# Optimization experiments

Hardware: AMD Instinct MI355X
Metric: run time of the kernel (lower is better)

The kernel has to match this reference:

```python
import jax, jax.numpy as jnp
import numpy as np
from jax import lax

N_HEAD = 16
SEQ = 2048
EMB = 512
D = SEQ // N_HEAD  # input_dim = 128
KSIZE = 3
EPS = 1e-5  # BatchNorm1d default eps


def setup_inputs() -> dict:
    key = jax.random.key(0)
    ks = jax.random.split(key, 5)
    inputs = jax.random.normal(ks[0], (8, SEQ, EMB), jnp.float32)
    # grouped Conv1d: groups = D, weight shape (out_ch, in_ch/groups, k) = (512, 4, 3)
    conv_w = jax.random.normal(ks[1], (EMB, EMB // D, KSIZE), jnp.float32) * 0.1
    conv_b = jax.random.normal(ks[2], (EMB,), jnp.float32) * 0.1
    gamma = jnp.ones((EMB,), jnp.float32)
    beta = jnp.zeros((EMB,), jnp.float32)
    lin_w = jax.random.normal(ks[3], (D, D), jnp.float32) * (1.0 / np.sqrt(D))
    lin_b = jax.random.normal(ks[4], (D,), jnp.float32) * 0.1
    return {"inputs": inputs, "conv_w": conv_w, "conv_b": conv_b,
            "gamma": gamma, "beta": beta, "lin_w": lin_w, "lin_b": lin_b}


def reference(inputs, conv_w, conv_b, gamma, beta, lin_w, lin_b):
    b = inputs.shape[0]
    # nlp mode: (b, S, E) -> (b*n_head, E, D)
    x = inputs.reshape(-1, EMB, D)

    # local information: grouped Conv1d (stride 1, padding 1, groups=D) + residual, GELU, BatchNorm (training stats)
    conv = lax.conv_general_dilated(
        x, conv_w, window_strides=(1,), padding=[(1, 1)],
        dimension_numbers=("NCH", "OIH", "NCH"), feature_group_count=D,
    ) + conv_b[None, :, None]
    q = jax.nn.gelu(conv + x, approximate=False)
    mu = q.mean(axis=(0, 2), keepdims=True)
    var = q.var(axis=(0, 2), keepdims=True)  # biased, as torch BN uses for normalization
    q = gamma[None, :, None] * (q - mu) * lax.rsqrt(var + EPS) + beta[None, :, None]

    # bernoulli sampling with prob=1 -> all-ones mask -> plain softmax over dim=-2 (the E axis)
    k = jax.nn.gelu(jax.nn.softmax(x, axis=1), approximate=False)

    # global information: Linear(D, D) on last dim, then GELU
    v = jax.nn.gelu(jnp.einsum("bed,od->beo", x, lin_w) + lin_b, approximate=False)

    # attention: (B', E, D) x (B', D, E) -> (B', E, E), softmax over last dim
    attn = jax.nn.softmax(
        jnp.einsum("bed,bfd->bef", q, k) / np.float32(np.sqrt(EMB)), axis=-1
    )
    out = jnp.einsum("bef,bfd->bed", attn, v)  # (B', E, D)
    return out.reshape(b, SEQ, EMB), attn
```

## Files before the change

### kernel.cpp

```cpp
#include <hip/hip_runtime.h>
#include <math.h>

#define Bn   128
#define Ech  512
#define Dd   128
#define NCNT 16384

typedef __bf16 bf16;
typedef __attribute__((ext_vector_type(8))) __bf16 bf16x8;
typedef __attribute__((ext_vector_type(4))) __bf16 bf16x4;
typedef __attribute__((ext_vector_type(4))) float f32x4;

__device__ __forceinline__ float gelu_exact(float x) {
    return 0.5f * x * (1.0f + erff(x * 0.70710678118654752f));
}

static __device__ __forceinline__ f32x4 mfma16(bf16x8 a, bf16x8 b, f32x4 c) {
    return __builtin_amdgcn_mfma_f32_16x16x32_bf16(a, b, c, 0, 0, 0);
}

#define SWZ(byte, row) ((unsigned)(byte) ^ (((unsigned)(row) & 7u) << 4))

__global__ __launch_bounds__(256) void k_conv_gelu_stats(
    const float* __restrict__ x, const float* __restrict__ cw,
    const float* __restrict__ cb, bf16* __restrict__ qpre,
    float* __restrict__ csum, float* __restrict__ csumsq)
{
    __shared__ float xt[64 * 128];
    const int n  = blockIdx.y;
    const int c0 = blockIdx.x * 64;
    const float* xb = x + (size_t)n * Ech * Dd + (size_t)c0 * Dd;

    const float4* xb4 = (const float4*)xb;
    float4* xt4 = (float4*)xt;
    #pragma unroll
    for (int j = 0; j < 8; j++) xt4[threadIdx.x + 256 * j] = xb4[threadIdx.x + 256 * j];
    __syncthreads();

    const int oloc = threadIdx.x >> 2;
    const int hq   = threadIdx.x & 3;
    const int o    = c0 + oloc;
    const int gb   = oloc & ~3;

    float w[4][3];
    #pragma unroll
    for (int i = 0; i < 4; i++)
        #pragma unroll
        for (int kk = 0; kk < 3; kk++) w[i][kk] = cw[o * 12 + i * 3 + kk];
    const float bias = cb[o];

    float s = 0.f, ss = 0.f;
    bf16* qrow = qpre + (size_t)n * Ech * Dd + (size_t)o * Dd;
    #pragma unroll 4
    for (int j = 0; j < 32; j++) {
        const int h = hq + 4 * j;
        float acc = bias;
        #pragma unroll
        for (int i = 0; i < 4; i++) {
            const float* row = &xt[(gb + i) * 128];
            const float xm = (h > 0)   ? row[h - 1] : 0.f;
            const float xc = row[h];
            const float xp = (h < 127) ? row[h + 1] : 0.f;
            acc = fmaf(xm, w[i][0], acc);
            acc = fmaf(xc, w[i][1], acc);
            acc = fmaf(xp, w[i][2], acc);
        }
        acc += xt[oloc * 128 + h];
        const float g = gelu_exact(acc);
        qrow[h] = (bf16)g;
        s += g; ss = fmaf(g, g, ss);
    }
    s  += __shfl_xor(s, 1);  s  += __shfl_xor(s, 2);
    ss += __shfl_xor(ss, 1); ss += __shfl_xor(ss, 2);
    if (hq == 0) { atomicAdd(&csum[o], s); atomicAdd(&csumsq[o], ss); }
}

__global__ void k_stats_final(const float* __restrict__ csum,
                              const float* __restrict__ csumsq,
                              const float* __restrict__ gamma,
                              const float* __restrict__ beta,
                              float* __restrict__ scale, float* __restrict__ shift)
{
    const int c = threadIdx.x;
    if (c < Ech) {
        const float mu   = csum[c]   * (1.0f / NCNT);
        const float var  = csumsq[c] * (1.0f / NCNT) - mu * mu;
        const float rstd = rsqrtf(var + 1e-5f);
        const float sc   = gamma[c] * rstd;
        scale[c] = sc;
        shift[c] = beta[c] - mu * sc;
    }
}

__global__ __launch_bounds__(256) void k_softmax_e_gelu_v2(
    const float* __restrict__ x, bf16* __restrict__ kout)
{
    __shared__ float4 red[32][8];
    const int n  = blockIdx.y;
    const int qd = blockIdx.x;
    const int t  = threadIdx.x;
    const int d4 = t & 7;
    const int eg = t >> 3;
    const float* xb = x + (size_t)n * Ech * Dd + qd * 32 + d4 * 4;

    float4 vb[16];
    float4 m4 = {-3e38f, -3e38f, -3e38f, -3e38f};
    #pragma unroll
    for (int j = 0; j < 16; j++) {
        const int e = eg + 32 * j;
        float4 v = *(const float4*)(xb + (size_t)e * Dd);
        vb[j] = v;
        m4.x = fmaxf(m4.x, v.x); m4.y = fmaxf(m4.y, v.y);
        m4.z = fmaxf(m4.z, v.z); m4.w = fmaxf(m4.w, v.w);
    }
    red[eg][d4] = m4;
    __syncthreads();
    #pragma unroll
    for (int s = 16; s >= 1; s >>= 1) {
        if (eg < s) {
            float4 a = red[eg][d4], b = red[eg + s][d4];
            a.x = fmaxf(a.x, b.x); a.y = fmaxf(a.y, b.y);
            a.z = fmaxf(a.z, b.z); a.w = fmaxf(a.w, b.w);
            red[eg][d4] = a;
        }
        __syncthreads();
    }
    m4 = red[0][d4];
    __syncthreads();

    float4 s4 = {0.f, 0.f, 0.f, 0.f};
    #pragma unroll
    for (int j = 0; j < 16; j++) {
        float4 v = vb[j];
        v.x = __expf(v.x - m4.x); v.y = __expf(v.y - m4.y);
        v.z = __expf(v.z - m4.z); v.w = __expf(v.w - m4.w);
        vb[j] = v;
        s4.x += v.x; s4.y += v.y; s4.z += v.z; s4.w += v.w;
    }
    red[eg][d4] = s4;
    __syncthreads();
    #pragma unroll
    for (int s = 16; s >= 1; s >>= 1) {
        if (eg < s) {
            float4 a = red[eg][d4], b = red[eg + s][d4];
            a.x += b.x; a.y += b.y; a.z += b.z; a.w += b.w;
            red[eg][d4] = a;
        }
        __syncthreads();
    }
    s4 = red[0][d4];
    const float4 inv4 = {1.0f / s4.x, 1.0f / s4.y, 1.0f / s4.z, 1.0f / s4.w};

    bf16* kb = kout + (size_t)n * Ech * Dd + qd * 32 + d4 * 4;
    #pragma unroll
    for (int j = 0; j < 16; j++) {
        const int e = eg + 32 * j;
        float4 p = vb[j];
        bf16x4 ov;
        ov[0] = (bf16)gelu_exact(p.x * inv4.x);
        ov[1] = (bf16)gelu_exact(p.y * inv4.y);
        ov[2] = (bf16)gelu_exact(p.z * inv4.z);
        ov[3] = (bf16)gelu_exact(p.w * inv4.w);
        *(bf16x4*)(kb + (size_t)e * Dd) = ov;
    }
}

__global__ __launch_bounds__(256) void k_vgemm_T(
    const float* __restrict__ x, const float* __restrict__ lw,
    const float* __restrict__ lb, bf16* __restrict__ vT)
{
    __shared__ bf16 As[64 * 128];
    __shared__ bf16 Bs[64 * 128];
    const int n = blockIdx.z, e0 = blockIdx.x * 64, o0 = blockIdx.y * 64;
    const int t = threadIdx.x, lane = t & 63, w = t >> 6;
    const int wr = w >> 1, wc = w & 1;
    const int lr = lane & 15, lg = lane >> 4;

    {
        const float* sa = lw + (size_t)o0 * Dd;
        const float* sb = x + (size_t)n * Ech * Dd + (size_t)e0 * Dd;
        #pragma unroll
        for (int p = 0; p < 4; p++) {
            const int idx = t + 256 * p;
            const int row = idx >> 4, k16 = idx & 15;
            float4 a0 = *(const float4*)(sa + (size_t)row * Dd + k16 * 8);
            float4 a1 = *(const float4*)(sa + (size_t)row * Dd + k16 * 8 + 4);
            bf16x8 oa;
            oa[0]=(bf16)a0.x; oa[1]=(bf16)a0.y; oa[2]=(bf16)a0.z; oa[3]=(bf16)a0.w;
            oa[4]=(bf16)a1.x; oa[5]=(bf16)a1.y; oa[6]=(bf16)a1.z; oa[7]=(bf16)a1.w;
            *(bf16x8*)((char*)As + SWZ(row * 256 + k16 * 16, row)) = oa;
            float4 b0 = *(const float4*)(sb + (size_t)row * Dd + k16 * 8);
            float4 b1 = *(const float4*)(sb + (size_t)row * Dd + k16 * 8 + 4);
            bf16x8 ob;
            ob[0]=(bf16)b0.x; ob[1]=(bf16)b0.y; ob[2]=(bf16)b0.z; ob[3]=(bf16)b0.w;
            ob[4]=(bf16)b1.x; ob[5]=(bf16)b1.y; ob[6]=(bf16)b1.z; ob[7]=(bf16)b1.w;
            *(bf16x8*)((char*)Bs + SWZ(row * 256 + k16 * 16, row)) = ob;
        }
    }
    __syncthreads();

    f32x4 acc[2][2] = {};
    #pragma unroll
    for (int ks = 0; ks < 4; ks++) {
        const int ko = ks * 32 + lg * 8;
        const int ra0 = wr * 32 + lr, ra1 = wr * 32 + 16 + lr;
        const int rb0 = wc * 32 + lr, rb1 = wc * 32 + 16 + lr;
        const bf16x8 a0 = *(const bf16x8*)((char*)As + SWZ(ra0 * 256 + ko * 2, ra0));
        const bf16x8 a1 = *(const bf16x8*)((char*)As + SWZ(ra1 * 256 + ko * 2, ra1));
        const bf16x8 b0 = *(const bf16x8*)((char*)Bs + SWZ(rb0 * 256 + ko * 2, rb0));
        const bf16x8 b1 = *(const bf16x8*)((char*)Bs + SWZ(rb1 * 256 + ko * 2, rb1));
        acc[0][0] = mfma16(a0, b0, acc[0][0]);
        acc[0][1] = mfma16(a0, b1, acc[0][1]);
        acc[1][0] = mfma16(a1, b0, acc[1][0]);
        acc[1][1] = mfma16(a1, b1, acc[1][1]);
    }

    bf16* vb = vT + (size_t)n * Dd * Ech;
    #pragma unroll
    for (int mm = 0; mm < 2; mm++) {
        #pragma unroll
        for (int nn = 0; nn < 2; nn++) {
            const int ecol = e0 + wc * 32 + nn * 16 + lr;
            #pragma unroll
            for (int r4 = 0; r4 < 4; r4++) {
                const int orow = o0 + wr * 32 + mm * 16 + lg * 4 + r4;
                vb[(size_t)orow * Ech + ecol] =
                    (bf16)gelu_exact(acc[mm][nn][r4] + lb[orow]);
            }
        }
    }
}

#define QS_OFF 0
#define KS_OFF 16384
#define PS_OFF 16384
#define VS_OFF 81920
#define LDS_TOTAL 147456

__global__ __launch_bounds__(256) void k_attn_fused(
    const bf16* __restrict__ qpre, const bf16* __restrict__ kbuf,
    const bf16* __restrict__ vT, const float* __restrict__ scale,
    const float* __restrict__ shift, float* __restrict__ attn,
    float* __restrict__ out)
{
    __shared__ char lds[LDS_TOTAL];
    const int n = blockIdx.y, e0 = blockIdx.x * 64;
    const int t = threadIdx.x, lane = t & 63, w = t >> 6;
    const int lr = lane & 15, lg = lane >> 4;

    {
        const bf16* src = qpre + (size_t)n * Ech * Dd + (size_t)e0 * Dd;
        #pragma unroll
        for (int p = 0; p < 4; p++) {
            const int idx = t + 256 * p;
            const int row = idx >> 4, k16 = idx & 15;
            bf16x8 v = *(const bf16x8*)(src + row * Dd + k16 * 8);
            const float sc = scale[e0 + row], sh = shift[e0 + row];
            bf16x8 o;
            #pragma unroll
            for (int j = 0; j < 8; j++) o[j] = (bf16)fmaf((float)v[j], sc, sh);
            *(bf16x8*)(lds + QS_OFF + SWZ(row * 256 + k16 * 16, row)) = o;
        }
    }
    {
        const bf16* src = kbuf + (size_t)n * Ech * Dd;
        #pragma unroll
        for (int p = 0; p < 32; p++) {
            const int idx = t + 256 * p;
            const int row = idx >> 4, k16 = idx & 15;
            float4 v = *(const float4*)(src + row * Dd + k16 * 8);
            *(float4*)(lds + KS_OFF + SWZ(row * 256 + k16 * 16, row)) = v;
        }
    }
    __syncthreads();

    f32x4 acc[32];
    #pragma unroll
    for (int i = 0; i < 32; i++) acc[i] = (f32x4){0.f, 0.f, 0.f, 0.f};
    #pragma unroll
    for (int ks = 0; ks < 4; ks++) {
        const int arow = w * 16 + lr;
        const int ko = ks * 32 + lg * 8;
        const bf16x8 a = *(const bf16x8*)(lds + QS_OFF + SWZ(arow * 256 + ko * 2, arow));
        #pragma unroll
        for (int ft = 0; ft < 32; ft++) {
            const int brow = ft * 16 + lr;
            const bf16x8 b = *(const bf16x8*)(lds + KS_OFF + SWZ(brow * 256 + ko * 2, brow));
            acc[ft] = mfma16(a, b, acc[ft]);
        }
    }
    __syncthreads();

    const float rsc = 0.044194173824159216f;
    float m[4] = {-3e38f, -3e38f, -3e38f, -3e38f};
    #pragma unroll
    for (int ft = 0; ft < 32; ft++)
        #pragma unroll
        for (int r4 = 0; r4 < 4; r4++) m[r4] = fmaxf(m[r4], acc[ft][r4]);
    #pragma unroll
    for (int off = 1; off <= 8; off <<= 1)
        #pragma unroll
        for (int r4 = 0; r4 < 4; r4++) m[r4] = fmaxf(m[r4], __shfl_xor(m[r4], off));

    float s[4] = {0.f, 0.f, 0.f, 0.f};
    #pragma unroll
    for (int ft = 0; ft < 32; ft++)
        #pragma unroll
        for (int r4 = 0; r4 < 4; r4++) {
            const float p = __expf((acc[ft][r4] - m[r4]) * rsc);
            acc[ft][r4] = p;
            s[r4] += p;
        }
    #pragma unroll
    for (int off = 1; off <= 8; off <<= 1)
        #pragma unroll
        for (int r4 = 0; r4 < 4; r4++) s[r4] += __shfl_xor(s[r4], off);
    float inv[4];
    #pragma unroll
    for (int r4 = 0; r4 < 4; r4++) inv[r4] = 1.0f / s[r4];

    #pragma unroll
    for (int ft = 0; ft < 32; ft++)
        #pragma unroll
        for (int r4 = 0; r4 < 4; r4++) {
            const int row = w * 16 + lg * 4 + r4;
            const int col = ft * 16 + lr;
            *(bf16*)(lds + PS_OFF + SWZ(row * 1024 + col * 2, row)) =
                (bf16)(acc[ft][r4] * inv[r4]);
        }

    const bf16* vsrc = vT + (size_t)n * Dd * Ech;
    #pragma unroll
    for (int p = 0; p < 16; p++) {
        const int idx = t + 256 * p;
        const int row = idx >> 5, c16 = idx & 31;
        float4 v = *(const float4*)(vsrc + (size_t)row * Ech + c16 * 8);
        *(float4*)(lds + VS_OFF + SWZ(row * 512 + c16 * 16, row)) = v;
    }
    __syncthreads();

    f32x4 acc2[8];
    #pragma unroll
    for (int i = 0; i < 8; i++) acc2[i] = (f32x4){0.f, 0.f, 0.f, 0.f};
    #pragma unroll
    for (int kf = 0; kf < 8; kf++) {
        const int arow = w * 16 + lr;
        const int fcol = kf * 32 + lg * 8;
        const bf16x8 a = *(const bf16x8*)(lds + PS_OFF + SWZ(arow * 1024 + fcol * 2, arow));
        #pragma unroll
        for (int dt = 0; dt < 8; dt++) {
            const int brow = dt * 16 + lr;
            const bf16x8 b = *(const bf16x8*)(lds + VS_OFF + SWZ(brow * 512 + fcol * 2, brow));
            acc2[dt] = mfma16(a, b, acc2[dt]);
        }
    }

    {
        float* ab = attn + (size_t)n * Ech * Ech + (size_t)e0 * Ech;
        #pragma unroll
        for (int p = 0; p < 32; p++) {
            const int idx = t + 256 * p;
            const int row = idx >> 7, c4 = idx & 127;
            bf16x4 pv = *(const bf16x4*)(lds + PS_OFF + SWZ(row * 1024 + c4 * 8, row));
            float4 o = {(float)pv[0], (float)pv[1], (float)pv[2], (float)pv[3]};
            *(float4*)(ab + (size_t)row * Ech + c4 * 4) = o;
        }
    }
    __syncthreads();

    #pragma unroll
    for (int p = 0; p < 16; p++) {
        const int idx = t + 256 * p;
        const int row = idx >> 5, c16 = idx & 31;
        float4 v = *(const float4*)(vsrc + (size_t)row * Ech + 256 + c16 * 8);
        *(float4*)(lds + VS_OFF + SWZ(row * 512 + c16 * 16, row)) = v;
    }
    __syncthreads();

    #pragma unroll
    for (int kf = 0; kf < 8; kf++) {
        const int arow = w * 16 + lr;
        const int fcol = 256 + kf * 32 + lg * 8;
        const bf16x8 a = *(const bf16x8*)(lds + PS_OFF + SWZ(arow * 1024 + fcol * 2, arow));
        #pragma unroll
        for (int dt = 0; dt < 8; dt++) {
            const int brow = dt * 16 + lr;
            const int vcol = kf * 32 + lg * 8;
            const bf16x8 b = *(const bf16x8*)(lds + VS_OFF + SWZ(brow * 512 + vcol * 2, brow));
            acc2[dt] = mfma16(a, b, acc2[dt]);
        }
    }

    float* ob = out + (size_t)n * Ech * Dd;
    #pragma unroll
    for (int dt = 0; dt < 8; dt++)
        #pragma unroll
        for (int r4 = 0; r4 < 4; r4++) {
            const int erow = e0 + w * 16 + lg * 4 + r4;
            const int dcol = dt * 16 + lr;
            ob[(size_t)erow * Dd + dcol] = acc2[dt][r4];
        }
}

extern "C" void kernel_launch(void* const* d_in, const int* in_sizes, int n_in,
                              void* d_out, int out_size, void* d_ws, size_t ws_size,
                              hipStream_t stream)
{
    const float* x     = (const float*)d_in[0];
    const float* cw    = (const float*)d_in[1];
    const float* cb    = (const float*)d_in[2];
    const float* gamma = (const float*)d_in[3];
    const float* beta  = (const float*)d_in[4];
    const float* lw    = (const float*)d_in[5];
    const float* lb    = (const float*)d_in[6];

    float* out  = (float*)d_out;
    float* attn = out + (size_t)8388608;

    bf16*  qpre_bf = (bf16*)d_ws;
    bf16*  kb_bf   = qpre_bf + 8388608;
    bf16*  vT_bf   = kb_bf + 8388608;
    float* csum    = (float*)(vT_bf + 8388608);
    float* csumsq  = csum + 512;
    float* scale   = csumsq + 512;
    float* shift   = scale + 512;

    hipMemsetAsync(csum, 0, 2 * 512 * sizeof(float), stream);

    k_conv_gelu_stats<<<dim3(8, 128), 256, 0, stream>>>(x, cw, cb, qpre_bf, csum, csumsq);
    k_stats_final<<<1, 512, 0, stream>>>(csum, csumsq, gamma, beta, scale, shift);
    k_softmax_e_gelu_v2<<<dim3(4, 128), 256, 0, stream>>>(x, kb_bf);
    k_vgemm_T<<<dim3(8, 2, 128), 256, 0, stream>>>(x, lw, lb, vT_bf);
    k_attn_fused<<<dim3(8, 128), 256, 0, stream>>>(
        qpre_bf, kb_bf, vT_bf, scale, shift, attn, out);
}
```

Baseline: 310.6 us.

## Restructure fused attention kernel into 2x2 warp tiling with smaller LDS footprint

The fused attention kernel now splits its four warps into a 2x2 grid. Each warp keeps its Q fragments in registers, streams K in two 256-row chunks, and merges softmax row max and sum across the two column-warps through a small LDS exchange. P reuses the K buffer, and V is streamed in 64-column chunks, which cuts LDS from 144KB to 80KB so more blocks can be resident per CU. In exchange the kernel has more barriers, a cross-warp softmax reduction, and loads Q directly from global memory.

```diff
diff --git a/kernel.cpp b/kernel.cpp
--- a/kernel.cpp
+++ b/kernel.cpp
@@ -231,129 +231,151 @@
     }
 }
 
-#define QS_OFF 0
-#define KS_OFF 16384
-#define PS_OFF 16384
-#define VS_OFF 81920
-#define LDS_TOTAL 147456
-
-__global__ __launch_bounds__(256) void k_attn_fused(
+#define KP_OFF  0
+#define SMR_OFF 65536
+#define VC_OFF  65536
+#define ATT_LDS 81920
+
+__global__ __launch_bounds__(256) void k_attn_fused2(
     const bf16* __restrict__ qpre, const bf16* __restrict__ kbuf,
     const bf16* __restrict__ vT, const float* __restrict__ scale,
     const float* __restrict__ shift, float* __restrict__ attn,
     float* __restrict__ out)
 {
-    __shared__ char lds[LDS_TOTAL];
+    __shared__ char lds[ATT_LDS];
     const int n = blockIdx.y, e0 = blockIdx.x * 64;
     const int t = threadIdx.x, lane = t & 63, w = t >> 6;
+    const int wr = w >> 1, wc = w & 1;
     const int lr = lane & 15, lg = lane >> 4;
 
-    {
-        const bf16* src = qpre + (size_t)n * Ech * Dd + (size_t)e0 * Dd;
-        #pragma unroll
-        for (int p = 0; p < 4; p++) {
+    bf16x8 qa[2][4];
+    #pragma unroll
+    for (int rt = 0; rt < 2; rt++) {
+        const int row = e0 + wr * 32 + rt * 16 + lr;
+        const float sc = scale[row], sh = shift[row];
+        const bf16* qr = qpre + (size_t)n * Ech * Dd + (size_t)row * Dd + lg * 8;
+        #pragma unroll
+        for (int ks = 0; ks < 4; ks++) {
+            bf16x8 v = *(const bf16x8*)(qr + ks * 32);
+            bf16x8 o;
+            #pragma unroll
+            for (int j = 0; j < 8; j++) o[j] = (bf16)fmaf((float)v[j], sc, sh);
+            qa[rt][ks] = o;
+        }
+    }
+
+    f32x4 acc[2][16];
+    #pragma unroll
+    for (int rt = 0; rt < 2; rt++)
+        #pragma unroll
+        for (int j = 0; j < 16; j++) acc[rt][j] = (f32x4){0.f, 0.f, 0.f, 0.f};
+
+    const bf16* kb = kbuf + (size_t)n * Ech * Dd;
+    #pragma unroll
+    for (int c = 0; c < 2; c++) {
+        __syncthreads();
+        #pragma unroll
+        for (int p = 0; p < 16; p++) {
             const int idx = t + 256 * p;
             const int row = idx >> 4, k16 = idx & 15;
-            bf16x8 v = *(const bf16x8*)(src + row * Dd + k16 * 8);
-            const float sc = scale[e0 + row], sh = shift[e0 + row];
-            bf16x8 o;
-            #pragma unroll
-            for (int j = 0; j < 8; j++) o[j] = (bf16)fmaf((float)v[j], sc, sh);
-            *(bf16x8*)(lds + QS_OFF + SWZ(row * 256 + k16 * 16, row)) = o;
-        }
-    }
-    {
-        const bf16* src = kbuf + (size_t)n * Ech * Dd;
-        #pragma unroll
-        for (int p = 0; p < 32; p++) {
-            const int idx = t + 256 * p;
-            const int row = idx >> 4, k16 = idx & 15;
-            float4 v = *(const float4*)(src + row * Dd + k16 * 8);
-            *(float4*)(lds + KS_OFF + SWZ(row * 256 + k16 * 16, row)) = v;
-        }
-    }
-    __syncthreads();
-
-    f32x4 acc[32];
-    #pragma unroll
-    for (int i = 0; i < 32; i++) acc[i] = (f32x4){0.f, 0.f, 0.f, 0.f};
-    #pragma unroll
-    for (int ks = 0; ks < 4; ks++) {
-        const int arow = w * 16 + lr;
-        const int ko = ks * 32 + lg * 8;
-        const bf16x8 a = *(const bf16x8*)(lds + QS_OFF + SWZ(arow * 256 + ko * 2, arow));
-        #pragma unroll
-        for (int ft = 0; ft < 32; ft++) {
-            const int brow = ft * 16 + lr;
-            const bf16x8 b = *(const bf16x8*)(lds + KS_OFF + SWZ(brow * 256 + ko * 2, brow));
-            acc[ft] = mfma16(a, b, acc[ft]);
-        }
-    }
-    __syncthreads();
+            float4 v = *(const float4*)(kb + (size_t)(c * 256 + row) * Dd + k16 * 8);
+            *(float4*)(lds + KP_OFF + SWZ(row * 256 + k16 * 16, row)) = v;
+        }
+        __syncthreads();
+        #pragma unroll
+        for (int ks = 0; ks < 4; ks++)
+            #pragma unroll
+            for (int ct = 0; ct < 8; ct++) {
+                const int brow = wc * 128 + ct * 16 + lr;
+                const bf16x8 b = *(const bf16x8*)(lds + KP_OFF +
+                                   SWZ(brow * 256 + ks * 64 + lg * 16, brow));
+                acc[0][c * 8 + ct] = mfma16(qa[0][ks], b, acc[0][c * 8 + ct]);
+                acc[1][c * 8 + ct] = mfma16(qa[1][ks], b, acc[1][c * 8 + ct]);
+            }
+    }
 
     const float rsc = 0.044194173824159216f;
-    float m[4] = {-3e38f, -3e38f, -3e38f, -3e38f};
-    #pragma unroll
-    for (int ft = 0; ft < 32; ft++)
-        #pragma unroll
-        for (int r4 = 0; r4 < 4; r4++) m[r4] = fmaxf(m[r4], acc[ft][r4]);
+    float mloc[2][4], sloc[2][4];
+    #pragma unroll
+    for (int rt = 0; rt < 2; rt++)
+        #pragma unroll
+        for (int r4 = 0; r4 < 4; r4++) mloc[rt][r4] = -3e38f;
+    #pragma unroll
+    for (int rt = 0; rt < 2; rt++)
+        #pragma unroll
+        for (int j = 0; j < 16; j++)
+            #pragma unroll
+            for (int r4 = 0; r4 < 4; r4++)
+                mloc[rt][r4] = fmaxf(mloc[rt][r4], acc[rt][j][r4]);
     #pragma unroll
     for (int off = 1; off <= 8; off <<= 1)
         #pragma unroll
-        for (int r4 = 0; r4 < 4; r4++) m[r4] = fmaxf(m[r4], __shfl_xor(m[r4], off));
-
-    float s[4] = {0.f, 0.f, 0.f, 0.f};
-    #pragma unroll
-    for (int ft = 0; ft < 32; ft++)
+        for (int rt = 0; rt < 2; rt++)
+            #pragma unroll
+            for (int r4 = 0; r4 < 4; r4++)
+                mloc[rt][r4] = fmaxf(mloc[rt][r4], __shfl_xor(mloc[rt][r4], off));
+
+    #pragma unroll
+    for (int rt = 0; rt < 2; rt++)
+        #pragma unroll
+        for (int r4 = 0; r4 < 4; r4++) sloc[rt][r4] = 0.f;
+    #pragma unroll
+    for (int rt = 0; rt < 2; rt++)
+        #pragma unroll
+        for (int j = 0; j < 16; j++)
+            #pragma unroll
+            for (int r4 = 0; r4 < 4; r4++) {
+                const float p = __expf((acc[rt][j][r4] - mloc[rt][r4]) * rsc);
+                acc[rt][j][r4] = p;
+                sloc[rt][r4] += p;
+            }
+    #pragma unroll
+    for (int off = 1; off <= 8; off <<= 1)
+        #pragma unroll
+        for (int rt = 0; rt < 2; rt++)
+            #pragma unroll
+            for (int r4 = 0; r4 < 4; r4++)
+                sloc[rt][r4] += __shfl_xor(sloc[rt][r4], off);
+
+    float* pmax = (float*)(lds + SMR_OFF);
+    float* psum = (float*)(lds + SMR_OFF + 512);
+    if (lr == 0) {
+        #pragma unroll
+        for (int rt = 0; rt < 2; rt++)
+            #pragma unroll
+            for (int r4 = 0; r4 < 4; r4++) {
+                const int row = wr * 32 + rt * 16 + lg * 4 + r4;
+                pmax[wc * 64 + row] = mloc[rt][r4];
+                psum[wc * 64 + row] = sloc[rt][r4];
+            }
+    }
+    __syncthreads();
+
+    float fac[2][4];
+    #pragma unroll
+    for (int rt = 0; rt < 2; rt++)
         #pragma unroll
         for (int r4 = 0; r4 < 4; r4++) {
-            const float p = __expf((acc[ft][r4] - m[r4]) * rsc);
-            acc[ft][r4] = p;
-            s[r4] += p;
-        }
-    #pragma unroll
-    for (int off = 1; off <= 8; off <<= 1)
-        #pragma unroll
-        for (int r4 = 0; r4 < 4; r4++) s[r4] += __shfl_xor(s[r4], off);
-    float inv[4];
-    #pragma unroll
-    for (int r4 = 0; r4 < 4; r4++) inv[r4] = 1.0f / s[r4];
-
-    #pragma unroll
-    for (int ft = 0; ft < 32; ft++)
-        #pragma unroll
-        for (int r4 = 0; r4 < 4; r4++) {
-            const int row = w * 16 + lg * 4 + r4;
-            const int col = ft * 16 + lr;
-            *(bf16*)(lds + PS_OFF + SWZ(row * 1024 + col * 2, row)) =
-                (bf16)(acc[ft][r4] * inv[r4]);
-        }
-
-    const bf16* vsrc = vT + (size_t)n * Dd * Ech;
-    #pragma unroll
-    for (int p = 0; p < 16; p++) {
-        const int idx = t + 256 * p;
-        const int row = idx >> 5, c16 = idx & 31;
-        float4 v = *(const float4*)(vsrc + (size_t)row * Ech + c16 * 8);
-        *(float4*)(lds + VS_OFF + SWZ(row * 512 + c16 * 16, row)) = v;
-    }
-    __syncthreads();
-
-    f32x4 acc2[8];
-    #pragma unroll
-    for (int i = 0; i < 8; i++) acc2[i] = (f32x4){0.f, 0.f, 0.f, 0.f};
-    #pragma unroll
-    for (int kf = 0; kf < 8; kf++) {
-        const int arow = w * 16 + lr;
-        const int fcol = kf * 32 + lg * 8;
-        const bf16x8 a = *(const bf16x8*)(lds + PS_OFF + SWZ(arow * 1024 + fcol * 2, arow));
-        #pragma unroll
-        for (int dt = 0; dt < 8; dt++) {
-            const int brow = dt * 16 + lr;
-            const bf16x8 b = *(const bf16x8*)(lds + VS_OFF + SWZ(brow * 512 + fcol * 2, brow));
-            acc2[dt] = mfma16(a, b, acc2[dt]);
-        }
-    }
+            const int row = wr * 32 + rt * 16 + lg * 4 + r4;
+            const float m0 = pmax[row], m1 = pmax[64 + row];
+            const float s0 = psum[row], s1 = psum[64 + row];
+            const float M  = fmaxf(m0, m1);
+            const float S  = s0 * __expf((m0 - M) * rsc) + s1 * __expf((m1 - M) * rsc);
+            fac[rt][r4] = __expf((mloc[rt][r4] - M) * rsc) / S;
+        }
+
+    #pragma unroll
+    for (int rt = 0; rt < 2; rt++)
+        #pragma unroll
+        for (int j = 0; j < 16; j++)
+            #pragma unroll
+            for (int r4 = 0; r4 < 4; r4++) {
+                const int row = wr * 32 + rt * 16 + lg * 4 + r4;
+                const int col = (j >> 3) * 256 + wc * 128 + (j & 7) * 16 + lr;
+                *(bf16*)(lds + KP_OFF + SWZ(row * 1024 + col * 2, row)) =
+                    (bf16)(acc[rt][j][r4] * fac[rt][r4]);
+            }
+    __syncthreads();
 
     {
         float* ab = attn + (size_t)n * Ech * Ech + (size_t)e0 * Ech;
@@ -361,45 +383,58 @@
         for (int p = 0; p < 32; p++) {
             const int idx = t + 256 * p;
             const int row = idx >> 7, c4 = idx & 127;
-            bf16x4 pv = *(const bf16x4*)(lds + PS_OFF + SWZ(row * 1024 + c4 * 8, row));
+            bf16x4 pv = *(const bf16x4*)(lds + KP_OFF + SWZ(row * 1024 + c4 * 8, row));
             float4 o = {(float)pv[0], (float)pv[1], (float)pv[2], (float)pv[3]};
             *(float4*)(ab + (size_t)row * Ech + c4 * 4) = o;
         }
     }
-    __syncthreads();
-
-    #pragma unroll
-    for (int p = 0; p < 16; p++) {
-        const int idx = t + 256 * p;
-        const int row = idx >> 5, c16 = idx & 31;
-        float4 v = *(const float4*)(vsrc + (size_t)row * Ech + 256 + c16 * 8);
-        *(float4*)(lds + VS_OFF + SWZ(row * 512 + c16 * 16, row)) = v;
-    }
-    __syncthreads();
-
-    #pragma unroll
-    for (int kf = 0; kf < 8; kf++) {
-        const int arow = w * 16 + lr;
-        const int fcol = 256 + kf * 32 + lg * 8;
-        const bf16x8 a = *(const bf16x8*)(lds + PS_OFF + SWZ(arow * 1024 + fcol * 2, arow));
-        #pragma unroll
-        for (int dt = 0; dt < 8; dt++) {
-            const int brow = dt * 16 + lr;
-            const int vcol = kf * 32 + lg * 8;
-            const bf16x8 b = *(const bf16x8*)(lds + VS_OFF + SWZ(brow * 512 + vcol * 2, brow));
-            acc2[dt] = mfma16(a, b, acc2[dt]);
+
+    const bf16* vsrc = vT + (size_t)n * Dd * Ech;
+    f32x4 acc2[2][4];
+    #pragma unroll
+    for (int rt = 0; rt < 2; rt++)
+        #pragma unroll
+        for (int dtt = 0; dtt < 4; dtt++) acc2[rt][dtt] = (f32x4){0.f, 0.f, 0.f, 0.f};
+
+    #pragma unroll
+    for (int fc = 0; fc < 8; fc++) {
+        __syncthreads();
+        #pragma unroll
+        for (int p = 0; p < 4; p++) {
+            const int idx = t + 256 * p;
+            const int row = idx >> 3, c16 = idx & 7;
+            float4 v = *(const float4*)(vsrc + (size_t)row * Ech + fc * 64 + c16 * 8);
+            *(float4*)(lds + VC_OFF + SWZ(row * 128 + c16 * 16, row)) = v;
+        }
+        __syncthreads();
+        #pragma unroll
+        for (int ks2 = 0; ks2 < 2; ks2++) {
+            const int fcol = fc * 64 + ks2 * 32 + lg * 8;
+            const int ar0 = wr * 32 + lr, ar1 = wr * 32 + 16 + lr;
+            const bf16x8 a0 = *(const bf16x8*)(lds + KP_OFF + SWZ(ar0 * 1024 + fcol * 2, ar0));
+            const bf16x8 a1 = *(const bf16x8*)(lds + KP_OFF + SWZ(ar1 * 1024 + fcol * 2, ar1));
+            #pragma unroll
+            for (int dtt = 0; dtt < 4; dtt++) {
+                const int brow = wc * 64 + dtt * 16 + lr;
+                const bf16x8 b = *(const bf16x8*)(lds + VC_OFF +
+                                   SWZ(brow * 128 + ks2 * 64 + lg * 16, brow));
+                acc2[0][dtt] = mfma16(a0, b, acc2[0][dtt]);
+                acc2[1][dtt] = mfma16(a1, b, acc2[1][dtt]);
+            }
         }
     }
 
     float* ob = out + (size_t)n * Ech * Dd;
     #pragma unroll
-    for (int dt = 0; dt < 8; dt++)
-        #pragma unroll
-        for (int r4 = 0; r4 < 4; r4++) {
-            const int erow = e0 + w * 16 + lg * 4 + r4;
-            const int dcol = dt * 16 + lr;
-            ob[(size_t)erow * Dd + dcol] = acc2[dt][r4];
-        }
+    for (int rt = 0; rt < 2; rt++)
+        #pragma unroll
+        for (int dtt = 0; dtt < 4; dtt++)
+            #pragma unroll
+            for (int r4 = 0; r4 < 4; r4++) {
+                const int erow = e0 + wr * 32 + rt * 16 + lg * 4 + r4;
+                const int dcol = wc * 64 + dtt * 16 + lr;
+                ob[(size_t)erow * Dd + dcol] = acc2[rt][dtt][r4];
+            }
 }
 
 extern "C" void kernel_launch(void* const* d_in, const int* in_sizes, int n_in,
@@ -431,6 +466,6 @@
     k_stats_final<<<1, 512, 0, stream>>>(csum, csumsq, gamma, beta, scale, shift);
     k_softmax_e_gelu_v2<<<dim3(4, 128), 256, 0, stream>>>(x, kb_bf);
     k_vgemm_T<<<dim3(8, 2, 128), 256, 0, stream>>>(x, lw, lb, vT_bf);
-    k_attn_fused<<<dim3(8, 128), 256, 0, stream>>>(
+    k_attn_fused2<<<dim3(8, 128), 256, 0, stream>>>(
         qpre_bf, kb_bf, vT_bf, scale, shift, attn, out);
 }
```

Measured after the change: 310.7 us. Within noise of the previous version (+0.0%).
